# Kernel tuning notes

Hardware: AMD Instinct MI355X
Metric: run time of the kernel (lower is better)

Reference implementation:

```python
import jax, jax.numpy as jnp
import numpy as np

DIM = 2560; HEADS = 20; HEAD_DIM = 128
N_EXP = 4; TOP_K = 2; HID = 6912; SHID = 3584
B = 1; S = 2048
EPS = 1e-6


def setup_inputs():
    key = jax.random.key(0)
    ks = jax.random.split(key, 16)
    r = lambda i, shape, s=0.02: jax.random.normal(ks[i], shape, jnp.float32) * s
    # rope as [1,S,1,HD/2,2,2] rotation matrices: [[cos,-sin],[sin,cos]]
    ang = jax.random.uniform(ks[0], (1, S, 1, HEAD_DIM // 2), jnp.float32) * (2.0 * np.pi)
    c, s_ = jnp.cos(ang), jnp.sin(ang)
    rope = jnp.stack([jnp.stack([c, -s_], -1), jnp.stack([s_, c], -1)], -2)
    return dict(
        hidden_states=jax.random.normal(ks[1], (B, S, DIM), jnp.float32),
        temb=jax.random.normal(ks[2], (B, DIM), jnp.float32),
        rope=rope,
        adaln_w=r(3, (6 * DIM, DIM)), adaln_b=jnp.zeros((6 * DIM,), jnp.float32),
        qkv_w=r(4, (3 * DIM, DIM)), qkv_b=jnp.zeros((3 * DIM,), jnp.float32),
        qn_w=jnp.ones((DIM,), jnp.float32), kn_w=jnp.ones((DIM,), jnp.float32),
        out_w=r(5, (DIM, DIM)), out_b=jnp.zeros((DIM,), jnp.float32),
        gate_w=r(6, (N_EXP, DIM), 1.0 / DIM ** 0.5),
        ew1=r(7, (N_EXP, HID, DIM)), ew2=r(8, (N_EXP, DIM, HID)), ew3=r(9, (N_EXP, HID, DIM)),
        sw1=r(10, (SHID, DIM)), sw2=r(11, (DIM, SHID)), sw3=r(12, (SHID, DIM)),
    )


def _layernorm(x):  # elementwise_affine=False, eps=1e-6
    m = x.mean(-1, keepdims=True)
    v = ((x - m) ** 2).mean(-1, keepdims=True)
    return (x - m) * jax.lax.rsqrt(v + EPS)


def _rmsnorm(x, w):  # DistributedRMSNorm, tp_size=1
    return x * jax.lax.rsqrt((x ** 2).mean(-1, keepdims=True) + EPS) * w


def _apply_rope(x, rope):  # x:[B,S,H,D], rope:[1,S,1,D/2,2,2]
    b, s, h, d = x.shape
    x_ = x.reshape(b, s, h, d // 2, 1, 2)
    out = rope[..., 0] * x_[..., 0] + rope[..., 1] * x_[..., 1]  # [B,S,H,D/2,2]
    return out.reshape(b, s, h, d)


def _swiglu(x, w1, w2, w3):
    return (jax.nn.silu(x @ w1.T) * (x @ w3.T)) @ w2.T


def _forward(hidden_states, temb, rope, adaln_w, adaln_b, qkv_w, qkv_b, qn_w, kn_w,
             out_w, out_b, gate_w, ew1, ew2, ew3, sw1, sw2, sw3):
    b, s, d = hidden_states.shape
    # adaLN modulation: SiLU -> Linear -> [:, None] -> chunk(6)
    mod = (jax.nn.silu(temb) @ adaln_w.T + adaln_b)[:, None, :]
    shift_msa, scale_msa, gate_msa, shift_mlp, scale_mlp, gate_mlp = jnp.split(mod, 6, axis=-1)
    # --- attention ---
    nh = _layernorm(hidden_states) * (1.0 + scale_msa) + shift_msa
    qkv = nh @ qkv_w.T + qkv_b
    q, k, v = jnp.split(qkv, 3, axis=-1)  # each [B,S,inner_dim]
    q = _rmsnorm(q, qn_w)  # RMS over full inner_dim (all heads)
    k = _rmsnorm(k, kn_w)
    q = q.reshape(b, s, HEADS, HEAD_DIM)
    k = k.reshape(b, s, HEADS, HEAD_DIM)
    v = v.reshape(b, s, HEADS, HEAD_DIM)
    q = _apply_rope(q, rope)
    k = _apply_rope(k, rope)
    attn = jnp.einsum('bqhd,bkhd->bhqk', q, k) * (HEAD_DIM ** -0.5)
    attn = jax.nn.softmax(attn, axis=-1)
    o = jnp.einsum('bhqk,bkhd->bqhd', attn, v).reshape(b, s, HEADS * HEAD_DIM)
    o = o @ out_w.T + out_b
    hidden_states = gate_msa * o + hidden_states
    # --- MoE SwiGLU feed-forward ---
    nh = _layernorm(hidden_states) * (1.0 + scale_mlp) + shift_mlp
    x = nh.reshape(-1, d)  # [T,d]
    scores = jax.nn.softmax(x @ gate_w.T, axis=-1)  # [T,E]
    tw, ti = jax.lax.top_k(scores, TOP_K)  # norm_topk_prob=False
    t = x.shape[0]
    wdense = jnp.zeros((t, N_EXP), x.dtype).at[jnp.arange(t)[:, None], ti].set(tw)
    y = jnp.zeros_like(x)
    for e in range(N_EXP):  # fixed small expert count
        y = y + wdense[:, e:e + 1] * _swiglu(x, ew1[e], ew2[e], ew3[e])
    y = y.reshape(b, s, d) + _swiglu(nh, sw1, sw2, sw3)  # shared experts on identity
    return gate_mlp * y + hidden_states


def reference(hidden_states, temb, rope, adaln_w, adaln_b, qkv_w, qkv_b, qn_w, kn_w,
              out_w, out_b, gate_w, ew1, ew2, ew3, sw1, sw2, sw3):
    return _forward(hidden_states, temb, rope, adaln_w, adaln_b, qkv_w, qkv_b, qn_w, kn_w,
                    out_w, out_b, gate_w, ew1, ew2, ew3, sw1, sw2, sw3)
```

## Files before the change

### kernel.cpp

```cpp
#include <hip/hip_runtime.h>

#define DIM 2560
#define T_TOK 2048
#define NHEADS 20
#define HD 128
#define HID_E 6912
#define SHID_E 3584
#define MPAD 5120

typedef _Float16 f16x8 __attribute__((ext_vector_type(8)));
typedef float f32x4 __attribute__((ext_vector_type(4)));
typedef unsigned short u16x8 __attribute__((ext_vector_type(8)));

#define MFMA16(a, b, c) __builtin_amdgcn_mfma_f32_16x16x32_f16((a), (b), (c), 0, 0, 0)

__device__ inline unsigned short f2h(float f) {
  return __builtin_bit_cast(unsigned short, (_Float16)f);
}
__device__ inline float h2f(unsigned short u) {
  return (float)__builtin_bit_cast(_Float16, u);
}
__device__ inline float wave_sum(float v) {
#pragma unroll
  for (int off = 32; off > 0; off >>= 1) v += __shfl_down(v, off, 64);
  return v;
}
__device__ inline void gld16(const void* g, void* l) {
  __builtin_amdgcn_global_load_lds((const __attribute__((address_space(1))) void*)g,
                                   (__attribute__((address_space(3))) void*)l, 16, 0, 0);
}


__global__ __launch_bounds__(256) void silu_k(const float* __restrict__ t,
                                              float* __restrict__ ss) {
  int i = blockIdx.x * 256 + threadIdx.x;
  if (i < DIM) {
    float v = t[i];
    ss[i] = v / (1.f + expf(-v));
  }
}

__global__ __launch_bounds__(256) void cvt_f16(const float* __restrict__ in,
                                               unsigned short* __restrict__ outp, int n8) {
  const int stride = gridDim.x * 256;
  for (int i = blockIdx.x * 256 + threadIdx.x; i < n8; i += stride) {
    float4 a = *(const float4*)(in + (size_t)i * 8);
    float4 b = *(const float4*)(in + (size_t)i * 8 + 4);
    u16x8 u;
    u[0] = f2h(a.x); u[1] = f2h(a.y); u[2] = f2h(a.z); u[3] = f2h(a.w);
    u[4] = f2h(b.x); u[5] = f2h(b.y); u[6] = f2h(b.z); u[7] = f2h(b.w);
    *(u16x8*)&outp[(size_t)i * 8] = u;
  }
}

__global__ __launch_bounds__(256) void cvt_pair(const float* __restrict__ w1,
                                                const float* __restrict__ w3,
                                                unsigned short* __restrict__ outp) {
  const int j = blockIdx.x;
  const int g = j >> 5, r = j & 31;
  const float* src = (r < 16) ? (w1 + (size_t)(g * 16 + r) * DIM)
                              : (w3 + (size_t)(g * 16 + (r & 15)) * DIM);
  unsigned short* dst = outp + (size_t)j * DIM;
  for (int i = threadIdx.x; i < 320; i += 256) {
    float4 a = *(const float4*)(src + i * 8);
    float4 b = *(const float4*)(src + i * 8 + 4);
    u16x8 u;
    u[0] = f2h(a.x); u[1] = f2h(a.y); u[2] = f2h(a.z); u[3] = f2h(a.w);
    u[4] = f2h(b.x); u[5] = f2h(b.y); u[6] = f2h(b.z); u[7] = f2h(b.w);
    *(u16x8*)&dst[i * 8] = u;
  }
}

__global__ __launch_bounds__(256) void adaln_gemv(const float* __restrict__ ss,
                                                  const float* __restrict__ W,
                                                  const float* __restrict__ bias,
                                                  float* __restrict__ mod) {
  const int lane = threadIdx.x & 63;
  const int j = blockIdx.x * 4 + (threadIdx.x >> 6);
  const float* wr = W + (size_t)j * DIM;
  float p = 0.f;
  for (int i = lane; i < 640; i += 64) {
    float4 w = *(const float4*)(wr + i * 4);
    float4 x = *(const float4*)(ss + i * 4);
    p += w.x * x.x + w.y * x.y + w.z * x.z + w.w * x.w;
  }
  p = wave_sum(p);
  if (lane == 0) mod[j] = p + bias[j];
}

__global__ __launch_bounds__(256) void ln_mod(const float* __restrict__ x,
                                              const float* __restrict__ shift,
                                              const float* __restrict__ scale,
                                              unsigned short* __restrict__ outp) {
  __shared__ float rbuf[8];
  const int t = blockIdx.x, tid = threadIdx.x, lane = tid & 63, wid = tid >> 6;
  const float* xr = x + (size_t)t * DIM;
  float s = 0.f, sq = 0.f;
  for (int i = tid; i < 640; i += 256) {
    float4 v = *(const float4*)(xr + i * 4);
    s += v.x + v.y + v.z + v.w;
    sq += v.x * v.x + v.y * v.y + v.z * v.z + v.w * v.w;
  }
  s = wave_sum(s);
  sq = wave_sum(sq);
  if (lane == 0) {
    rbuf[wid] = s;
    rbuf[4 + wid] = sq;
  }
  __syncthreads();
  float S = rbuf[0] + rbuf[1] + rbuf[2] + rbuf[3];
  float SQ = rbuf[4] + rbuf[5] + rbuf[6] + rbuf[7];
  float mean = S * (1.f / DIM);
  float rs = rsqrtf(SQ * (1.f / DIM) - mean * mean + 1e-6f);
  for (int i = tid; i < 640; i += 256) {
    float4 v = *(const float4*)(xr + i * 4);
    float4 sc4 = *(const float4*)(scale + i * 4);
    float4 sh4 = *(const float4*)(shift + i * 4);
    ushort4 u;
    u.x = f2h((v.x - mean) * rs * (1.f + sc4.x) + sh4.x);
    u.y = f2h((v.y - mean) * rs * (1.f + sc4.y) + sh4.y);
    u.z = f2h((v.z - mean) * rs * (1.f + sc4.z) + sh4.z);
    u.w = f2h((v.w - mean) * rs * (1.f + sc4.w) + sh4.w);
    *(ushort4*)&outp[(size_t)t * DIM + i * 4] = u;
  }
}

__global__ __launch_bounds__(256) void rmsrope(const unsigned short* __restrict__ qkv,
                                               const float* __restrict__ qn,
                                               const float* __restrict__ kn,
                                               const float* __restrict__ rope,
                                               unsigned short* __restrict__ qh,
                                               unsigned short* __restrict__ kh) {
  __shared__ float rbuf[8];
  const int t = blockIdx.x, tid = threadIdx.x, lane = tid & 63, wid = tid >> 6;
  const unsigned short* row = qkv + (size_t)t * 7680;
  float sq = 0.f, sk = 0.f;
  for (int i = tid; i < 320; i += 256) {
    f16x8 qv = *(const f16x8*)(row + i * 8);
    f16x8 kv = *(const f16x8*)(row + DIM + i * 8);
#pragma unroll
    for (int j = 0; j < 8; ++j) {
      float q = (float)qv[j], k = (float)kv[j];
      sq += q * q;
      sk += k * k;
    }
  }
  sq = wave_sum(sq);
  sk = wave_sum(sk);
  if (lane == 0) {
    rbuf[wid] = sq;
    rbuf[4 + wid] = sk;
  }
  __syncthreads();
  float SQ = rbuf[0] + rbuf[1] + rbuf[2] + rbuf[3];
  float SK = rbuf[4] + rbuf[5] + rbuf[6] + rbuf[7];
  float rq = rsqrtf(SQ * (1.f / DIM) + 1e-6f) * 0.08838834764831845f;
  float rk = rsqrtf(SK * (1.f / DIM) + 1e-6f);
  for (int pp = tid; pp < 1280; pp += 256) {
    int c = pp * 2;
    float qe = h2f(row[c]) * rq * qn[c], qo = h2f(row[c + 1]) * rq * qn[c + 1];
    float ke = h2f(row[DIM + c]) * rk * kn[c], ko = h2f(row[DIM + c + 1]) * rk * kn[c + 1];
    float4 rr = *(const float4*)(rope + (size_t)t * 256 + (pp & 63) * 4);
    unsigned qp = (unsigned)f2h(rr.x * qe + rr.y * qo) |
                  ((unsigned)f2h(rr.z * qe + rr.w * qo) << 16);
    unsigned kp = (unsigned)f2h(rr.x * ke + rr.y * ko) |
                  ((unsigned)f2h(rr.z * ke + rr.w * ko) << 16);
    *(unsigned*)&qh[(size_t)t * DIM + c] = qp;
    *(unsigned*)&kh[(size_t)t * DIM + c] = kp;
  }
}

__global__ void transpose_v(const unsigned short* __restrict__ in,
                            unsigned short* __restrict__ outp) {
  __shared__ unsigned short tile[32][33];
  const int bx = blockIdx.x * 32;
  const int by = blockIdx.y * 32;
  const int tx = threadIdx.x, ty = threadIdx.y;
  for (int j = ty; j < 32; j += 8)
    tile[j][tx] = in[(size_t)(by + j) * 7680 + 5120 + bx + tx];
  __syncthreads();
  for (int j = ty; j < 32; j += 8)
    outp[(size_t)(bx + j) * T_TOK + by + tx] = tile[tx][j];
}

__global__ __launch_bounds__(256) void fattn(const unsigned short* __restrict__ qh,
                                             const unsigned short* __restrict__ kh,
                                             const unsigned short* __restrict__ vt,
                                             unsigned short* __restrict__ obuf) {
  __shared__ unsigned short sK[64 * 128];
  __shared__ unsigned short sV[128 * 64];
  __shared__ unsigned short sP[64 * 64];
  __shared__ float sRedM[4][64];
  __shared__ float sRedL[4][64];
  __shared__ float sM[64];
  __shared__ float sL[64];
  const int tid = threadIdx.x, lane = tid & 63, wv = tid >> 6;
  const int g = lane >> 4, fr = lane & 15;
  const int h = blockIdx.y;
  const int q0 = blockIdx.x * 64;

  {
    const int r = tid >> 2, qt = tid & 3;
    const unsigned short* gp = qh + (size_t)(q0 + r) * DIM + h * HD + qt * 32;
    uint4 v0 = ((const uint4*)gp)[0];
    uint4 v1 = ((const uint4*)gp)[1];
    uint4 v2 = ((const uint4*)gp)[2];
    uint4 v3 = ((const uint4*)gp)[3];
    unsigned short* dst = &sK[r * 128];
    const int cb = qt * 4, rs = r & 15;
    *(uint4*)&dst[((cb + 0) ^ rs) * 8] = v0;
    *(uint4*)&dst[((cb + 1) ^ rs) * 8] = v1;
    *(uint4*)&dst[((cb + 2) ^ rs) * 8] = v2;
    *(uint4*)&dst[((cb + 3) ^ rs) * 8] = v3;
  }
  __syncthreads();
  f16x8 qfrag[4][4];
#pragma unroll
  for (int ni = 0; ni < 4; ++ni) {
#pragma unroll
    for (int kt = 0; kt < 4; ++kt) {
      int r = ni * 16 + fr;
      qfrag[ni][kt] = *(const f16x8*)&sK[r * 128 + (((kt * 4 + g) ^ (r & 15)) << 3)];
    }
  }
  __syncthreads();

  f32x4 acco[4][2];
  f32x4 mprev[4];
  float mrun[4], lrun[4];
#pragma unroll
  for (int i = 0; i < 4; ++i) {
    acco[i][0] = (f32x4)0.f;
    acco[i][1] = (f32x4)0.f;
    mprev[i] = (f32x4)(-1e30f);
    mrun[i] = -1e30f;
    lrun[i] = 0.f;
  }

  for (int kt0 = 0; kt0 < T_TOK; kt0 += 64) {
    {
      const int r = tid >> 2, qt = tid & 3;
      const unsigned short* gp = kh + (size_t)(kt0 + r) * DIM + h * HD + qt * 32;
      uint4 v0 = ((const uint4*)gp)[0];
      uint4 v1 = ((const uint4*)gp)[1];
      uint4 v2 = ((const uint4*)gp)[2];
      uint4 v3 = ((const uint4*)gp)[3];
      unsigned short* dst = &sK[r * 128];
      const int cb = qt * 4, rs = r & 15;
      *(uint4*)&dst[((cb + 0) ^ rs) * 8] = v0;
      *(uint4*)&dst[((cb + 1) ^ rs) * 8] = v1;
      *(uint4*)&dst[((cb + 2) ^ rs) * 8] = v2;
      *(uint4*)&dst[((cb + 3) ^ rs) * 8] = v3;
      const int rv = tid >> 1, hf = tid & 1;
      const unsigned short* gv = vt + (size_t)(h * HD + rv) * T_TOK + kt0 + hf * 32;
      uint4 w0 = ((const uint4*)gv)[0];
      uint4 w1 = ((const uint4*)gv)[1];
      uint4 w2 = ((const uint4*)gv)[2];
      uint4 w3 = ((const uint4*)gv)[3];
      unsigned short* dv = &sV[rv * 64];
      const int cv = hf * 4, rvs = rv & 7;
      *(uint4*)&dv[((cv + 0) ^ rvs) * 8] = w0;
      *(uint4*)&dv[((cv + 1) ^ rvs) * 8] = w1;
      *(uint4*)&dv[((cv + 2) ^ rvs) * 8] = w2;
      *(uint4*)&dv[((cv + 3) ^ rvs) * 8] = w3;
    }
    __syncthreads();

    f32x4 accs[4] = {(f32x4)0.f, (f32x4)0.f, (f32x4)0.f, (f32x4)0.f};
#pragma unroll
    for (int kt = 0; kt < 4; ++kt) {
      int r = wv * 16 + fr;
      f16x8 ak = *(const f16x8*)&sK[r * 128 + (((kt * 4 + g) ^ (r & 15)) << 3)];
#pragma unroll
      for (int ni = 0; ni < 4; ++ni) accs[ni] = MFMA16(ak, qfrag[ni][kt], accs[ni]);
    }

    float pm[4];
#pragma unroll
    for (int ni = 0; ni < 4; ++ni) {
      float m = fmaxf(fmaxf(accs[ni][0], accs[ni][1]), fmaxf(accs[ni][2], accs[ni][3]));
      m = fmaxf(m, __shfl_xor(m, 16));
      m = fmaxf(m, __shfl_xor(m, 32));
      pm[ni] = m;
    }
    if (g == 0) {
#pragma unroll
      for (int ni = 0; ni < 4; ++ni) sRedM[wv][ni * 16 + fr] = pm[ni];
    }
    __syncthreads();
    float mnew[4];
#pragma unroll
    for (int ni = 0; ni < 4; ++ni) {
      int q = ni * 16 + fr;
      float mt = fmaxf(fmaxf(sRedM[0][q], sRedM[1][q]), fmaxf(sRedM[2][q], sRedM[3][q]));
      mnew[ni] = fmaxf(mrun[ni], mt);
    }
    float lsum[4];
#pragma unroll
    for (int ni = 0; ni < 4; ++ni) {
      float l0 = 0.f;
#pragma unroll
      for (int i = 0; i < 4; ++i) {
        float p = __expf(accs[ni][i] - mnew[ni]);
        accs[ni][i] = p;
        l0 += p;
      }
      l0 += __shfl_xor(l0, 16);
      l0 += __shfl_xor(l0, 32);
      lsum[ni] = l0;
    }
    if (g == 0) {
#pragma unroll
      for (int ni = 0; ni < 4; ++ni) sRedL[wv][ni * 16 + fr] = lsum[ni];
      if (wv == 0) {
#pragma unroll
        for (int ni = 0; ni < 4; ++ni) sM[ni * 16 + fr] = mnew[ni];
      }
    }
#pragma unroll
    for (int ni = 0; ni < 4; ++ni) {
      int q = ni * 16 + fr;
      unsigned p01 = (unsigned)f2h(accs[ni][0]) | ((unsigned)f2h(accs[ni][1]) << 16);
      unsigned p23 = (unsigned)f2h(accs[ni][2]) | ((unsigned)f2h(accs[ni][3]) << 16);
      uint2 pk;
      pk.x = p01;
      pk.y = p23;
      *(uint2*)&sP[q * 64 + ((((wv << 1) | (g >> 1)) ^ (q & 7)) << 3) + ((g & 1) << 2)] = pk;
    }
    __syncthreads();
#pragma unroll
    for (int ni = 0; ni < 4; ++ni) {
      int q = ni * 16 + fr;
      float lt = sRedL[0][q] + sRedL[1][q] + sRedL[2][q] + sRedL[3][q];
      lrun[ni] = lrun[ni] * __expf(mrun[ni] - mnew[ni]) + lt;
      mrun[ni] = mnew[ni];
    }

#pragma unroll
    for (int mi = 0; mi < 4; ++mi) {
      f32x4 mn = *(const f32x4*)&sM[mi * 16 + g * 4];
      f32x4 sc;
#pragma unroll
      for (int i = 0; i < 4; ++i) sc[i] = __expf(mprev[mi][i] - mn[i]);
      acco[mi][0] *= sc;
      acco[mi][1] *= sc;
      mprev[mi] = mn;
    }
#pragma unroll
    for (int ktp = 0; ktp < 2; ++ktp) {
      f16x8 bv[2];
#pragma unroll
      for (int nd = 0; nd < 2; ++nd) {
        int r = wv * 32 + nd * 16 + fr;
        bv[nd] = *(const f16x8*)&sV[r * 64 + (((ktp * 4 + g) ^ (r & 7)) << 3)];
      }
#pragma unroll
      for (int mi = 0; mi < 4; ++mi) {
        int r = mi * 16 + fr;
        f16x8 ap = *(const f16x8*)&sP[r * 64 + (((ktp * 4 + g) ^ (r & 7)) << 3)];
        acco[mi][0] = MFMA16(ap, bv[0], acco[mi][0]);
        acco[mi][1] = MFMA16(ap, bv[1], acco[mi][1]);
      }
    }
    __syncthreads();
  }

  if (wv == 0 && g == 0) {
#pragma unroll
    for (int ni = 0; ni < 4; ++ni) sL[ni * 16 + fr] = 1.f / lrun[ni];
  }
  __syncthreads();
#pragma unroll
  for (int mi = 0; mi < 4; ++mi) {
    f32x4 li = *(const f32x4*)&sL[mi * 16 + g * 4];
#pragma unroll
    for (int nd = 0; nd < 2; ++nd) {
#pragma unroll
      for (int i = 0; i < 4; ++i) {
        float o = acco[mi][nd][i] * li[i];
        obuf[(size_t)(q0 + mi * 16 + g * 4 + i) * DIM + h * HD + wv * 32 + nd * 16 + fr] =
            f2h(o);
      }
    }
  }
}

__global__ __launch_bounds__(256) void ln2_route(const float* __restrict__ x,
                                                 const float* __restrict__ shift,
                                                 const float* __restrict__ scale,
                                                 const float* __restrict__ gw,
                                                 unsigned short* __restrict__ nh2,
                                                 float* __restrict__ wd) {
  __shared__ float rbuf[8];
  __shared__ float gbuf[4][4];
  const int t = blockIdx.x, tid = threadIdx.x, lane = tid & 63, wid = tid >> 6;
  const float* xr = x + (size_t)t * DIM;
  float s = 0.f, sq = 0.f;
  for (int i = tid; i < 640; i += 256) {
    float4 v = *(const float4*)(xr + i * 4);
    s += v.x + v.y + v.z + v.w;
    sq += v.x * v.x + v.y * v.y + v.z * v.z + v.w * v.w;
  }
  s = wave_sum(s);
  sq = wave_sum(sq);
  if (lane == 0) {
    rbuf[wid] = s;
    rbuf[4 + wid] = sq;
  }
  __syncthreads();
  float S = rbuf[0] + rbuf[1] + rbuf[2] + rbuf[3];
  float SQ = rbuf[4] + rbuf[5] + rbuf[6] + rbuf[7];
  float mean = S * (1.f / DIM);
  float rs = rsqrtf(SQ * (1.f / DIM) - mean * mean + 1e-6f);
  float g0 = 0.f, g1 = 0.f, g2 = 0.f, g3 = 0.f;
  for (int i = tid; i < 640; i += 256) {
    float4 v = *(const float4*)(xr + i * 4);
    float4 sc4 = *(const float4*)(scale + i * 4);
    float4 sh4 = *(const float4*)(shift + i * 4);
    float y0 = (v.x - mean) * rs * (1.f + sc4.x) + sh4.x;
    float y1 = (v.y - mean) * rs * (1.f + sc4.y) + sh4.y;
    float y2 = (v.z - mean) * rs * (1.f + sc4.z) + sh4.z;
    float y3 = (v.w - mean) * rs * (1.f + sc4.w) + sh4.w;
    ushort4 u;
    u.x = f2h(y0); u.y = f2h(y1); u.z = f2h(y2); u.w = f2h(y3);
    *(ushort4*)&nh2[(size_t)t * DIM + i * 4] = u;
    float4 w0 = *(const float4*)(gw + i * 4);
    float4 w1 = *(const float4*)(gw + DIM + i * 4);
    float4 w2 = *(const float4*)(gw + 2 * DIM + i * 4);
    float4 w3 = *(const float4*)(gw + 3 * DIM + i * 4);
    g0 += y0 * w0.x + y1 * w0.y + y2 * w0.z + y3 * w0.w;
    g1 += y0 * w1.x + y1 * w1.y + y2 * w1.z + y3 * w1.w;
    g2 += y0 * w2.x + y1 * w2.y + y2 * w2.z + y3 * w2.w;
    g3 += y0 * w3.x + y1 * w3.y + y2 * w3.z + y3 * w3.w;
  }
  g0 = wave_sum(g0);
  g1 = wave_sum(g1);
  g2 = wave_sum(g2);
  g3 = wave_sum(g3);
  if (lane == 0) {
    gbuf[wid][0] = g0; gbuf[wid][1] = g1; gbuf[wid][2] = g2; gbuf[wid][3] = g3;
  }
  __syncthreads();
  if (tid == 0) {
    float l[4];
#pragma unroll
    for (int e = 0; e < 4; ++e) l[e] = gbuf[0][e] + gbuf[1][e] + gbuf[2][e] + gbuf[3][e];
    float mx = fmaxf(fmaxf(l[0], l[1]), fmaxf(l[2], l[3]));
    float ex[4], sum = 0.f;
#pragma unroll
    for (int e = 0; e < 4; ++e) { ex[e] = expf(l[e] - mx); sum += ex[e]; }
    float p[4];
#pragma unroll
    for (int e = 0; e < 4; ++e) p[e] = ex[e] / sum;
    int i1 = 0;
    for (int e = 1; e < 4; ++e)
      if (p[e] > p[i1]) i1 = e;
    int i2 = -1;
    for (int e = 0; e < 4; ++e) {
      if (e == i1) continue;
      if (i2 < 0 || p[e] > p[i2]) i2 = e;
    }
    float w[4] = {0.f, 0.f, 0.f, 0.f};
    w[i1] = p[i1];
    w[i2] = p[i2];
    *(float4*)&wd[(size_t)t * 4] = make_float4(w[0], w[1], w[2], w[3]);
  }
}

__global__ __launch_bounds__(256) void route_compact(const float* __restrict__ wd,
                                                     int* __restrict__ idx_all,
                                                     int* __restrict__ seg,
                                                     int* __restrict__ slotAB,
                                                     float* __restrict__ wAB) {
  __shared__ unsigned short c[256][4];
  __shared__ int offs[256][4];
  __shared__ int segs[5];
  const int t = threadIdx.x;
  for (int i = t; i < MPAD; i += 256) idx_all[i] = 0;
  unsigned char sel[8];
  float wv4[8][4];
  unsigned short lc[4] = {0, 0, 0, 0};
#pragma unroll
  for (int k = 0; k < 8; ++k) {
    int tok = t * 8 + k;
    float4 w = *(const float4*)&wd[(size_t)tok * 4];
    wv4[k][0] = w.x; wv4[k][1] = w.y; wv4[k][2] = w.z; wv4[k][3] = w.w;
    unsigned m = 0;
    if (w.x != 0.f) { m |= 1; lc[0]++; }
    if (w.y != 0.f) { m |= 2; lc[1]++; }
    if (w.z != 0.f) { m |= 4; lc[2]++; }
    if (w.w != 0.f) { m |= 8; lc[3]++; }
    sel[k] = (unsigned char)m;
  }
#pragma unroll
  for (int e = 0; e < 4; ++e) c[t][e] = lc[e];
  __syncthreads();
  if (t == 0) {
    int run[4] = {0, 0, 0, 0};
    for (int i = 0; i < 256; ++i) {
#pragma unroll
      for (int e = 0; e < 4; ++e) {
        offs[i][e] = run[e];
        run[e] += c[i][e];
      }
    }
    int s = 0;
    segs[0] = 0;
#pragma unroll
    for (int e = 0; e < 4; ++e) {
      s += (run[e] + 255) & ~255;
      segs[e + 1] = s;
    }
#pragma unroll
    for (int e = 0; e < 5; ++e) seg[e] = segs[e];
  }
  __syncthreads();
  int o[4];
#pragma unroll
  for (int e = 0; e < 4; ++e) o[e] = segs[e] + offs[t][e];
#pragma unroll
  for (int k = 0; k < 8; ++k) {
    int tok = t * 8 + k;
    unsigned m = sel[k];
    int sl[2] = {0, 0};
    float sw[2] = {0.f, 0.f};
    int ns = 0;
#pragma unroll
    for (int e = 0; e < 4; ++e) {
      if ((m >> e) & 1) {
        if (ns < 2) { sl[ns] = o[e]; sw[ns] = wv4[k][e]; }
        idx_all[o[e]++] = tok;
        ns++;
      }
    }
    if (ns == 1) { sl[1] = sl[0]; sw[1] = 0.f; }
    slotAB[tok * 2] = sl[0];
    slotAB[tok * 2 + 1] = sl[1];
    wAB[tok * 2] = sw[0];
    wAB[tok * 2 + 1] = sw[1];
  }
}

template <int EPI, int MODE>
__global__ __launch_bounds__(256) void gemm128(
    const unsigned short* __restrict__ A, const unsigned short* __restrict__ B,
    const float* __restrict__ bias, void* __restrict__ Cv,
    const float* __restrict__ aux0, const float* __restrict__ aux1,
    const int* __restrict__ idx, const int* __restrict__ seg,
    const int* __restrict__ slotAB, const float* __restrict__ wAB,
    const unsigned short* __restrict__ yc, int M, int N, int K) {
  __shared__ unsigned short smem[16384];
  const int tid = threadIdx.x;
  const int lane = tid & 63;
  const int wv = tid >> 6;
  const int nwg = gridDim.x;
  const int bid = blockIdx.x;
  const int swzb = (bid & 7) * (nwg >> 3) + (bid >> 3);
  const int gm = M >> 7;
  const int m0 = (swzb % gm) * 128, n0 = (swzb / gm) * 128;
  if (MODE != 0 && m0 >= seg[4]) return;

  const unsigned short* Bp = B;
  if constexpr (MODE != 0) {
    int e = 0;
#pragma unroll
    for (int i = 1; i < 4; ++i)
      if (m0 >= seg[i]) e = i;
    Bp = B + (size_t)e * N * K;
  }

  const int wm = (wv >> 1) * 64, wn = (wv & 1) * 64;
  const int fr = lane & 15, fc = lane >> 4;

  const int rl = lane >> 2, ch = lane & 3;
  const int R1 = wv * 16 + rl;
  const int R2 = 64 + R1;
  const int co1 = ((ch ^ ((R1 >> 1) & 3)) << 3);
  const int co2 = ((ch ^ ((R2 >> 1) & 3)) << 3);
  const size_t ar1 = (size_t)(m0 + R1) * K;
  const size_t ar2 = (size_t)(m0 + R2) * K;
  const unsigned short* gA1 = A + ar1 + co1;
  const unsigned short* gA2 = A + ar2 + co2;
  const unsigned short* gB1 = Bp + (size_t)(n0 + R1) * K + co1;
  const unsigned short* gB2 = Bp + (size_t)(n0 + R2) * K + co2;
  const int lA1 = (wv * 16) * 32, lA2 = (64 + wv * 16) * 32;

  f32x4 acc[4][4];
#pragma unroll
  for (int i = 0; i < 4; ++i) {
#pragma unroll
    for (int j = 0; j < 4; ++j) acc[i][j] = (f32x4)0.f;
  }

  auto STAGE = [&](int buf, int kt) {
    unsigned short* base = smem + buf * 8192;
    gld16(gA1 + kt, base + lA1);
    gld16(gA2 + kt, base + lA2);
    gld16(gB1 + kt, base + 4096 + lA1);
    gld16(gB2 + kt, base + 4096 + lA2);
  };
  auto COMPUTE = [&](int buf) {
    const unsigned short* sA = smem + buf * 8192;
    const unsigned short* sB = sA + 4096;
    f16x8 a[4], b[4];
#pragma unroll
    for (int mi = 0; mi < 4; ++mi) {
      int r = wm + mi * 16 + fr;
      a[mi] = *(const f16x8*)&sA[r * 32 + ((fc ^ ((r >> 1) & 3)) << 3)];
    }
#pragma unroll
    for (int ni = 0; ni < 4; ++ni) {
      int r = wn + ni * 16 + fr;
      b[ni] = *(const f16x8*)&sB[r * 32 + ((fc ^ ((r >> 1) & 3)) << 3)];
    }
#pragma unroll
    for (int mi = 0; mi < 4; ++mi) {
#pragma unroll
      for (int ni = 0; ni < 4; ++ni) acc[mi][ni] = MFMA16(a[mi], b[ni], acc[mi][ni]);
    }
  };

  const int nk = K >> 5;
  STAGE(0, 0);
  __syncthreads();
  int cur = 0;
  for (int t = 1; t < nk; ++t) {
    STAGE(cur ^ 1, t << 5);
    COMPUTE(cur);
    __syncthreads();
    cur ^= 1;
  }
  COMPUTE(cur);

#pragma unroll
  for (int mi = 0; mi < 4; ++mi) {
#pragma unroll
    for (int ni = 0; ni < 4; ++ni) {
      const int n = n0 + wn + ni * 16 + fr;
      const int mb = m0 + wm + mi * 16 + fc * 4;
#pragma unroll
      for (int i = 0; i < 4; ++i) {
        const int m = mb + i;
        float v = acc[mi][ni][i];
        const size_t cidx = (size_t)m * N + n;
        if constexpr (EPI == 1) {
          ((float*)Cv)[cidx] = aux0[n] * (v + bias[n]) + aux1[cidx];
        } else if constexpr (EPI == 4) {
          if (bias) v += bias[n];
          ((unsigned short*)Cv)[cidx] = f2h(v);
        } else if constexpr (EPI == 6) {
          const int sA_ = slotAB[m * 2], sB_ = slotAB[m * 2 + 1];
          const float wA_ = wAB[m * 2], wB_ = wAB[m * 2 + 1];
          float vm = wA_ * h2f(yc[(size_t)sA_ * N + n]) + wB_ * h2f(yc[(size_t)sB_ * N + n]);
          ((float*)Cv)[cidx] = aux0[n] * (v + vm) + aux1[cidx];
        }
      }
    }
  }
}

template <int EPI, int MODE>
__global__ __launch_bounds__(512) void gemm256(
    const unsigned short* __restrict__ A, const unsigned short* __restrict__ B,
    const float* __restrict__ bias, void* __restrict__ Cv,
    const int* __restrict__ idx, const int* __restrict__ seg,
    int M, int N, int K) {
  __shared__ unsigned short smem[32768];
  const int tid = threadIdx.x;
  const int lane = tid & 63;
  const int wv = tid >> 6;
  const int wr = wv >> 2;
  const int wc = wv & 3;
  const int fr = lane & 15, fc = lane >> 4;

  const int nwg = gridDim.x;
  const int bid = blockIdx.x;
  const int swzb = (bid & 7) * (nwg >> 3) + (bid >> 3);
  const int gm = M >> 8;
  const int m0 = (swzb % gm) * 256, n0 = (swzb / gm) * 256;
  if (MODE != 0 && m0 >= seg[4]) return;

  const unsigned short* Bp = B;
  if constexpr (MODE != 0) {
    int e = 0;
#pragma unroll
    for (int i = 1; i < 4; ++i)
      if (m0 >= seg[i]) e = i;
    Bp = B + (size_t)e * N * K;
  }

  const int srow = (lane >> 2);
  const int srcc = ((lane & 3) ^ ((lane >> 3) & 3)) << 3;
  int mr0, mr1;
  if constexpr (MODE == 1) {
    mr0 = idx[m0 + wv * 16 + srow];
    mr1 = idx[m0 + 128 + wv * 16 + srow];
  } else {
    mr0 = m0 + wv * 16 + srow;
    mr1 = m0 + 128 + wv * 16 + srow;
  }
  const unsigned short* gA0 = A + (size_t)mr0 * K + srcc;
  const unsigned short* gA1 = A + (size_t)mr1 * K + srcc;
  const unsigned short* gB0 = Bp + (size_t)(n0 + wv * 16 + srow) * K + srcc;
  const unsigned short* gB1 = Bp + (size_t)(n0 + 128 + wv * 16 + srow) * K + srcc;
  const int lw = wv << 9;

  const int sw = (fr >> 1) & 3;
  const int fo = ((fc ^ sw) << 3);
  const int aoff = (wr * 128 + fr) * 32 + fo;
  const int boff = (wc * 64 + fr) * 32 + fo;

  f32x4 acc[8][4];
#pragma unroll
  for (int i = 0; i < 8; ++i) {
#pragma unroll
    for (int j = 0; j < 4; ++j) acc[i][j] = (f32x4)0.f;
  }

  const int nk = K >> 5;
  gld16(gA0, &smem[lw]);
  gld16(gA1, &smem[4096 + lw]);
  gld16(gB0, &smem[8192 + lw]);
  gld16(gB1, &smem[12288 + lw]);
  __syncthreads();

  for (int t = 0; t < nk; ++t) {
    const int cb = (t & 1) * 16384;
    const int nb = cb ^ 16384;
    const int kn = (t + 1) << 5;
    const bool more = (t + 1) < nk;
    const unsigned short* sA = smem + cb;
    const unsigned short* sB = smem + cb + 8192;

    f16x8 b0 = *(const f16x8*)&sB[boff];
    f16x8 b1 = *(const f16x8*)&sB[boff + 512];
    f16x8 b2 = *(const f16x8*)&sB[boff + 1024];
    f16x8 b3 = *(const f16x8*)&sB[boff + 1536];
    {
      f16x8 a0 = *(const f16x8*)&sA[aoff];
      f16x8 a1 = *(const f16x8*)&sA[aoff + 512];
      if (more) {
        gld16(gA0 + kn, &smem[nb + lw]);
        gld16(gA1 + kn, &smem[nb + 4096 + lw]);
      }
      __builtin_amdgcn_sched_barrier(0);
      __builtin_amdgcn_s_setprio(1);
      acc[0][0] = MFMA16(a0, b0, acc[0][0]);
      acc[0][1] = MFMA16(a0, b1, acc[0][1]);
      acc[0][2] = MFMA16(a0, b2, acc[0][2]);
      acc[0][3] = MFMA16(a0, b3, acc[0][3]);
      acc[1][0] = MFMA16(a1, b0, acc[1][0]);
      acc[1][1] = MFMA16(a1, b1, acc[1][1]);
      acc[1][2] = MFMA16(a1, b2, acc[1][2]);
      acc[1][3] = MFMA16(a1, b3, acc[1][3]);
      __builtin_amdgcn_s_setprio(0);
      __builtin_amdgcn_sched_barrier(0);
    }
    {
      f16x8 a0 = *(const f16x8*)&sA[aoff + 1024];
      f16x8 a1 = *(const f16x8*)&sA[aoff + 1536];
      if (more) {
        gld16(gB0 + kn, &smem[nb + 8192 + lw]);
        gld16(gB1 + kn, &smem[nb + 12288 + lw]);
      }
      __builtin_amdgcn_sched_barrier(0);
      __builtin_amdgcn_s_setprio(1);
      acc[2][0] = MFMA16(a0, b0, acc[2][0]);
      acc[2][1] = MFMA16(a0, b1, acc[2][1]);
      acc[2][2] = MFMA16(a0, b2, acc[2][2]);
      acc[2][3] = MFMA16(a0, b3, acc[2][3]);
      acc[3][0] = MFMA16(a1, b0, acc[3][0]);
      acc[3][1] = MFMA16(a1, b1, acc[3][1]);
      acc[3][2] = MFMA16(a1, b2, acc[3][2]);
      acc[3][3] = MFMA16(a1, b3, acc[3][3]);
      __builtin_amdgcn_s_setprio(0);
      __builtin_amdgcn_sched_barrier(0);
    }
    {
      f16x8 a0 = *(const f16x8*)&sA[aoff + 2048];
      f16x8 a1 = *(const f16x8*)&sA[aoff + 2560];
      __builtin_amdgcn_sched_barrier(0);
      __builtin_amdgcn_s_setprio(1);
      acc[4][0] = MFMA16(a0, b0, acc[4][0]);
      acc[4][1] = MFMA16(a0, b1, acc[4][1]);
      acc[4][2] = MFMA16(a0, b2, acc[4][2]);
      acc[4][3] = MFMA16(a0, b3, acc[4][3]);
      acc[5][0] = MFMA16(a1, b0, acc[5][0]);
      acc[5][1] = MFMA16(a1, b1, acc[5][1]);
      acc[5][2] = MFMA16(a1, b2, acc[5][2]);
      acc[5][3] = MFMA16(a1, b3, acc[5][3]);
      __builtin_amdgcn_s_setprio(0);
      __builtin_amdgcn_sched_barrier(0);
    }
    {
      f16x8 a0 = *(const f16x8*)&sA[aoff + 3072];
      f16x8 a1 = *(const f16x8*)&sA[aoff + 3584];
      __builtin_amdgcn_sched_barrier(0);
      __builtin_amdgcn_s_setprio(1);
      acc[6][0] = MFMA16(a0, b0, acc[6][0]);
      acc[6][1] = MFMA16(a0, b1, acc[6][1]);
      acc[6][2] = MFMA16(a0, b2, acc[6][2]);
      acc[6][3] = MFMA16(a0, b3, acc[6][3]);
      acc[7][0] = MFMA16(a1, b0, acc[7][0]);
      acc[7][1] = MFMA16(a1, b1, acc[7][1]);
      acc[7][2] = MFMA16(a1, b2, acc[7][2]);
      acc[7][3] = MFMA16(a1, b3, acc[7][3]);
      __builtin_amdgcn_s_setprio(0);
      __builtin_amdgcn_sched_barrier(0);
    }
    __syncthreads();
  }

  if constexpr (EPI == 5) {
    unsigned short* Ch = (unsigned short*)Cv;
    const int Nh = N >> 1;
#pragma unroll
    for (int mi = 0; mi < 8; ++mi) {
#pragma unroll
      for (int p = 0; p < 2; ++p) {
        const int hcol = (((n0 + wc * 64) >> 5) + p) * 16 + fr;
        const int mb = m0 + wr * 128 + mi * 16 + fc * 4;
#pragma unroll
        for (int i = 0; i < 4; ++i) {
          const int m = mb + i;
          float v1 = acc[mi][2 * p][i];
          float v3 = acc[mi][2 * p + 1][i];
          float y = v1 / (1.f + __expf(-v1)) * v3;
          Ch[(size_t)m * Nh + hcol] = f2h(y);
        }
      }
    }
  } else {
    unsigned short* Ch = (unsigned short*)Cv;
#pragma unroll
    for (int mi = 0; mi < 8; ++mi) {
#pragma unroll
      for (int ni = 0; ni < 4; ++ni) {
        const int n = n0 + wc * 64 + ni * 16 + fr;
        const int mb = m0 + wr * 128 + mi * 16 + fc * 4;
#pragma unroll
        for (int i = 0; i < 4; ++i) {
          const int m = mb + i;
          float v = acc[mi][ni][i];
          if (bias) v += bias[n];
          Ch[(size_t)m * N + n] = f2h(v);
        }
      }
    }
  }
}


extern "C" void kernel_launch(void* const* d_in, const int* in_sizes, int n_in,
                              void* d_out, int out_size, void* d_ws, size_t ws_size,
                              hipStream_t stream) {
  (void)in_sizes; (void)n_in; (void)out_size; (void)ws_size;
  const float* hs = (const float*)d_in[0];
  const float* temb = (const float*)d_in[1];
  const float* rope = (const float*)d_in[2];
  const float* adaw = (const float*)d_in[3];
  const float* adab = (const float*)d_in[4];
  const float* qkvw = (const float*)d_in[5];
  const float* qkvb = (const float*)d_in[6];
  const float* qnw = (const float*)d_in[7];
  const float* knw = (const float*)d_in[8];
  const float* outw = (const float*)d_in[9];
  const float* outb = (const float*)d_in[10];
  const float* gatew = (const float*)d_in[11];
  const float* ew1 = (const float*)d_in[12];
  const float* ew2 = (const float*)d_in[13];
  const float* ew3 = (const float*)d_in[14];
  const float* sw1 = (const float*)d_in[15];
  const float* sw2 = (const float*)d_in[16];
  const float* sw3 = (const float*)d_in[17];
  float* out = (float*)d_out;
  char* ws = (char*)d_ws;

  size_t off = 0;
  auto give = [&](size_t nbytes) {
    size_t r = off;
    off += (nbytes + 255) & ~(size_t)255;
    return r;
  };
  const size_t T = T_TOK, D = DIM;
  size_t o_mod = give(15360 * 4);
  size_t o_ss = give(D * 4);
  size_t o_wd = give(T * 4 * 4);
  size_t o_idx = give(MPAD * 4);
  size_t o_seg = give(8 * 4);
  size_t o_slot = give(T * 2 * 4);
  size_t o_wab = give(T * 2 * 4);
  size_t o_nh = give(T * D * 2);
  size_t o_qkvh = give(T * 7680 * 2);
  size_t o_qh = give(T * D * 2);
  size_t o_kh = give(T * D * 2);
  size_t o_vt = give(T * D * 2);
  size_t o_obf = give(T * D * 2);
  size_t o_h2 = give(T * D * 4);
  size_t o_yc = give((size_t)MPAD * D * 2);
  size_t o_hmid2 = give(T * SHID_E * 2);
  size_t o_qkvw = give((size_t)7680 * 2560 * 2);
  size_t o_outw = give((size_t)2560 * 2560 * 2);
  size_t o_ewA = give((size_t)4 * 2 * HID_E * 2560 * 2);
  size_t o_ew2 = give((size_t)4 * 2560 * HID_E * 2);
  size_t o_swA = give((size_t)2 * SHID_E * 2560 * 2);
  size_t o_sw2 = give((size_t)2560 * SHID_E * 2);

  float* mod = (float*)(ws + o_mod);
  float* ss = (float*)(ws + o_ss);
  float* wd = (float*)(ws + o_wd);
  int* idxb = (int*)(ws + o_idx);
  int* segp = (int*)(ws + o_seg);
  int* slotAB = (int*)(ws + o_slot);
  float* wAB = (float*)(ws + o_wab);
  unsigned short* nh_h = (unsigned short*)(ws + o_nh);
  unsigned short* qkvh = (unsigned short*)(ws + o_qkvh);
  unsigned short* qh = (unsigned short*)(ws + o_qh);
  unsigned short* kh = (unsigned short*)(ws + o_kh);
  unsigned short* vt = (unsigned short*)(ws + o_vt);
  unsigned short* obf = (unsigned short*)(ws + o_obf);
  float* h2 = (float*)(ws + o_h2);
  unsigned short* yc = (unsigned short*)(ws + o_yc);
  unsigned short* hmid2 = (unsigned short*)(ws + o_hmid2);
  unsigned short* qkvw_h = (unsigned short*)(ws + o_qkvw);
  unsigned short* outw_h = (unsigned short*)(ws + o_outw);
  unsigned short* ewA_h = (unsigned short*)(ws + o_ewA);
  unsigned short* ew2_h = (unsigned short*)(ws + o_ew2);
  unsigned short* swA_h = (unsigned short*)(ws + o_swA);
  unsigned short* sw2_h = (unsigned short*)(ws + o_sw2);
  unsigned short* nh2 = nh_h;
  unsigned short* hmid = qkvh;

  cvt_f16<<<2048, 256, 0, stream>>>(qkvw, qkvw_h, 7680 * 2560 / 8);
  cvt_f16<<<2048, 256, 0, stream>>>(outw, outw_h, 2560 * 2560 / 8);
  cvt_f16<<<2048, 256, 0, stream>>>(ew2, ew2_h, 4 * 2560 * HID_E / 8);
  cvt_f16<<<2048, 256, 0, stream>>>(sw2, sw2_h, 2560 * SHID_E / 8);
  for (int e = 0; e < 4; ++e) {
    cvt_pair<<<2 * HID_E, 256, 0, stream>>>(ew1 + (size_t)e * HID_E * DIM,
                                            ew3 + (size_t)e * HID_E * DIM,
                                            ewA_h + (size_t)e * 2 * HID_E * DIM);
  }
  cvt_pair<<<2 * SHID_E, 256, 0, stream>>>(sw1, sw3, swA_h);
  silu_k<<<10, 256, 0, stream>>>(temb, ss);
  adaln_gemv<<<3840, 256, 0, stream>>>(ss, adaw, adab, mod);
  ln_mod<<<T, 256, 0, stream>>>(hs, mod, mod + D, nh_h);
  gemm256<4, 0><<<240, 512, 0, stream>>>(nh_h, qkvw_h, qkvb, qkvh,
                                         nullptr, nullptr, 2048, 7680, 2560);
  rmsrope<<<T, 256, 0, stream>>>(qkvh, qnw, knw, rope, qh, kh);
  transpose_v<<<dim3(80, 64), dim3(32, 8), 0, stream>>>(qkvh, vt);
  fattn<<<dim3(32, 20), 256, 0, stream>>>(qh, kh, vt, obf);
  gemm128<1, 0><<<16 * 20, 256, 0, stream>>>(obf, outw_h, outb, h2,
                                             mod + 2 * D, hs, nullptr, nullptr,
                                             nullptr, nullptr, nullptr, 2048, 2560, 2560);
  ln2_route<<<T, 256, 0, stream>>>(h2, mod + 3 * D, mod + 4 * D, gatew, nh2, wd);
  route_compact<<<1, 256, 0, stream>>>(wd, idxb, segp, slotAB, wAB);
  gemm256<5, 1><<<20 * 54, 512, 0, stream>>>(nh2, ewA_h, nullptr, hmid,
                                             idxb, segp, MPAD, 2 * HID_E, 2560);
  gemm128<4, 2><<<40 * 20, 256, 0, stream>>>(hmid, ew2_h, nullptr, yc,
                                             nullptr, nullptr, nullptr, segp,
                                             nullptr, nullptr, nullptr,
                                             MPAD, 2560, 6912);
  gemm256<5, 0><<<8 * 28, 512, 0, stream>>>(nh2, swA_h, nullptr, hmid2,
                                            nullptr, nullptr, 2048, 2 * SHID_E, 2560);
  gemm128<6, 0><<<16 * 20, 256, 0, stream>>>(hmid2, sw2_h, nullptr, out,
                                             mod + 5 * D, h2, nullptr, nullptr,
                                             slotAB, wAB, yc, 2048, 2560, 3584);
}
```

Baseline: 1.487 ms.

## Triple-buffer gemm256 shared-memory tiles with prefetch two K-steps ahead

The 256x256 GEMM moves from double-buffered to triple-buffered LDS. It prefetches tiles two K-steps ahead and waits with a manual vmcnt(4) plus a single barrier per iteration instead of two __syncthreads. The aim is to hide global-load latency behind more MFMA work and to cut barrier overhead. The cost is 96KB of LDS per block, which lowers occupancy, and the explicit vmcnt counting is fragile: it depends on four outstanding loads per thread per stage. Correctness at the start of each iteration relies on the single barrier ensuring all waves have finished reading the buffer that is about to be overwritten.

```diff
diff --git a/kernel.cpp b/kernel.cpp
--- a/kernel.cpp
+++ b/kernel.cpp
@@ -665,7 +665,7 @@
     const float* __restrict__ bias, void* __restrict__ Cv,
     const int* __restrict__ idx, const int* __restrict__ seg,
     int M, int N, int K) {
-  __shared__ unsigned short smem[32768];
+  __shared__ unsigned short smem[49152];
   const int tid = threadIdx.x;
   const int lane = tid & 63;
   const int wv = tid >> 6;
@@ -722,15 +722,27 @@
   gld16(gA1, &smem[4096 + lw]);
   gld16(gB0, &smem[8192 + lw]);
   gld16(gB1, &smem[12288 + lw]);
-  __syncthreads();
-
+  gld16(gA0 + 32, &smem[16384 + lw]);
+  gld16(gA1 + 32, &smem[16384 + 4096 + lw]);
+  gld16(gB0 + 32, &smem[16384 + 8192 + lw]);
+  gld16(gB1 + 32, &smem[16384 + 12288 + lw]);
+
+  int cur = 0;
   for (int t = 0; t < nk; ++t) {
-    const int cb = (t & 1) * 16384;
-    const int nb = cb ^ 16384;
-    const int kn = (t + 1) << 5;
-    const bool more = (t + 1) < nk;
-    const unsigned short* sA = smem + cb;
-    const unsigned short* sB = smem + cb + 8192;
+    if (t < nk - 1)
+      asm volatile("s_waitcnt vmcnt(4)" ::: "memory");
+    else
+      asm volatile("s_waitcnt vmcnt(0)" ::: "memory");
+    __builtin_amdgcn_s_barrier();
+    __builtin_amdgcn_sched_barrier(0);
+
+    const unsigned short* sA = smem + cur * 16384;
+    const unsigned short* sB = sA + 8192;
+    int nxt = cur + 2;
+    if (nxt >= 3) nxt -= 3;
+    unsigned short* nbase = smem + nxt * 16384;
+    const bool more = (t + 2) < nk;
+    const int kn = (t + 2) << 5;
 
     f16x8 b0 = *(const f16x8*)&sB[boff];
     f16x8 b1 = *(const f16x8*)&sB[boff + 512];
@@ -740,8 +752,8 @@
       f16x8 a0 = *(const f16x8*)&sA[aoff];
       f16x8 a1 = *(const f16x8*)&sA[aoff + 512];
       if (more) {
-        gld16(gA0 + kn, &smem[nb + lw]);
-        gld16(gA1 + kn, &smem[nb + 4096 + lw]);
+        gld16(gA0 + kn, nbase + lw);
+        gld16(gA1 + kn, nbase + 4096 + lw);
       }
       __builtin_amdgcn_sched_barrier(0);
       __builtin_amdgcn_s_setprio(1);
@@ -760,8 +772,8 @@
       f16x8 a0 = *(const f16x8*)&sA[aoff + 1024];
       f16x8 a1 = *(const f16x8*)&sA[aoff + 1536];
       if (more) {
-        gld16(gB0 + kn, &smem[nb + 8192 + lw]);
-        gld16(gB1 + kn, &smem[nb + 12288 + lw]);
+        gld16(gB0 + kn, nbase + 8192 + lw);
+        gld16(gB1 + kn, nbase + 12288 + lw);
       }
       __builtin_amdgcn_sched_barrier(0);
       __builtin_amdgcn_s_setprio(1);
@@ -808,7 +820,8 @@
       __builtin_amdgcn_s_setprio(0);
       __builtin_amdgcn_sched_barrier(0);
     }
-    __syncthreads();
+    cur += 1;
+    if (cur >= 3) cur -= 3;
   }
 
   if constexpr (EPI == 5) {
```

After: 1.423 ms. -4.3%, faster.
